# Kernel tuning notes

Hardware: AMD Instinct MI355X
Metric: run time of the kernel (lower is better)

Reference implementation:

```python
import jax, jax.numpy as jnp
import numpy as np

N = 50000      # nodes
DEG = 16       # fixed neighbor count per node -> E = N*DEG edges
F_IN = 128
F_OUT = 128


def setup_inputs() -> dict:
    key = jax.random.key(0)
    k = jax.random.split(key, 6)
    E = N * DEG
    x = jax.random.normal(k[0], (N, F_IN), dtype=jnp.float32)
    weight = jax.random.normal(k[1], (F_IN, F_OUT), dtype=jnp.float32) * (1.0 / np.sqrt(F_OUT))
    bias = jax.random.normal(k[2], (F_OUT,), dtype=jnp.float32) * (1.0 / np.sqrt(F_OUT))
    weights_mask = jax.random.normal(k[3], (2 * F_IN, F_IN), dtype=jnp.float32) * (1.0 / np.sqrt(F_IN))
    adj_vals = jax.random.uniform(k[4], (E,), dtype=jnp.float32)
    edge_src = jax.random.randint(k[5], (E,), 0, N, dtype=jnp.int32)   # neighbor ids (add_all flattened)
    edge_dst = jnp.repeat(jnp.arange(N, dtype=jnp.int32), DEG)         # center node ids
    return {"x": x, "weight": weight, "bias": bias, "weights_mask": weights_mask,
            "adj_vals": adj_vals, "edge_src": edge_src, "edge_dst": edge_dst}


def reference(x, weight, bias, weights_mask, adj_vals, edge_src, edge_dst):
    # Per-edge: concat(center, neighbor) -> mask MLP -> sigmoid (dropout omitted: eval mode)
    cen = x[edge_dst]                    # [E, F]
    nei = x[edge_src]                    # [E, F]
    cen_nei = jnp.concatenate([cen, nei], axis=1)          # [E, 2F]
    mask = jax.nn.sigmoid(cen_nei @ weights_mask)          # [E, F]
    # Weighted neighbor sum scattered back to centers, plus self feature
    agg = jax.ops.segment_sum(mask * nei, edge_dst, num_segments=N)   # [N, F]
    x_new = x + agg
    # Dense transform then spmm aggregation (adj given as edge list with values)
    support = x_new @ weight                                # [N, F_out]
    out = jax.ops.segment_sum(adj_vals[:, None] * support[edge_src], edge_dst, num_segments=N)
    return out + bias
```

## Files before the change

kernel.cpp:

```cpp
#include <hip/hip_runtime.h>
#include <stdint.h>
#include <stddef.h>


#define NNODES 50000
#define DEG    16
#define FD     128

#define NEG_LOG2E -1.44269504f

typedef __bf16 bf16x8 __attribute__((ext_vector_type(8)));
typedef short  s16x8  __attribute__((ext_vector_type(8)));
typedef float  f32x4  __attribute__((ext_vector_type(4)));
typedef float  f32x2  __attribute__((ext_vector_type(2)));

__device__ __forceinline__ short f2bf_s(float f) {
    union { float f; uint32_t u; } v; v.f = f;
    uint32_t r = v.u + 0x7fffu + ((v.u >> 16) & 1u);
    return (short)(r >> 16);
}
__device__ __forceinline__ float bflo(uint32_t u) {
    union { uint32_t u; float f; } v; v.u = u << 16;
    return v.f;
}
__device__ __forceinline__ float bfhi(uint32_t u) {
    union { uint32_t u; float f; } v; v.u = u & 0xffff0000u;
    return v.f;
}
__device__ __forceinline__ uint32_t pkbf(float lo, float hi) {
    return (uint32_t)(uint16_t)f2bf_s(lo) | ((uint32_t)(uint16_t)f2bf_s(hi) << 16);
}

__global__ __launch_bounds__(256) void pack_k(const float* __restrict__ wm,
                                              const float* __restrict__ w,
                                              short* __restrict__ wmb,
                                              short* __restrict__ wpack) {
    int tid = blockIdx.x * 256 + threadIdx.x;
    if (tid < 128 * 256) {
        int k = tid >> 8, c = tid & 255;
        float v = (c < 128) ? wm[k * 128 + c] : wm[(128 + k) * 128 + (c - 128)];
        int idx = (((k >> 5) * 16 + (c >> 4)) * 64 + ((k >> 3) & 3) * 16 + (c & 15)) * 8 + (k & 7);
        wmb[idx] = f2bf_s(NEG_LOG2E * v);
    }
    if (tid < 128 * 128) {
        int k = tid >> 7, n = tid & 127;
        int idx = (((k >> 5) * 8 + (n >> 4)) * 64 + ((k >> 3) & 3) * 16 + (n & 15)) * 8 + (k & 7);
        wpack[idx] = f2bf_s(w[tid]);
    }
}

__global__ __launch_bounds__(256) void zy_k(const float* __restrict__ x,
                                            const short* __restrict__ wmb,
                                            short* __restrict__ ezb,
                                            uint32_t* __restrict__ xb,
                                            uint8_t* __restrict__ y8) {
    __shared__ float ct[16 * 260];
    const int tid = threadIdx.x, wave = tid >> 6, lane = tid & 63;
    const int q = lane >> 4, m = lane & 15;
    const int node0 = blockIdx.x * 16;

    f32x4 acc[4];
    #pragma unroll
    for (int nt = 0; nt < 4; ++nt) acc[nt] = (f32x4){0.f, 0.f, 0.f, 0.f};

    #pragma unroll
    for (int kk = 0; kk < 4; ++kk) {
        const float* rp = x + (size_t)(node0 + m) * FD + kk * 32 + q * 8;
        f32x4 lo = *reinterpret_cast<const f32x4*>(rp);
        f32x4 hi = *reinterpret_cast<const f32x4*>(rp + 4);
        bf16x8 a;
        a[0]=(__bf16)lo.x; a[1]=(__bf16)lo.y; a[2]=(__bf16)lo.z; a[3]=(__bf16)lo.w;
        a[4]=(__bf16)hi.x; a[5]=(__bf16)hi.y; a[6]=(__bf16)hi.z; a[7]=(__bf16)hi.w;
        #pragma unroll
        for (int nt = 0; nt < 4; ++nt) {
            int frag = kk * 16 + wave * 4 + nt;
            s16x8 braw = *reinterpret_cast<const s16x8*>(wmb + ((size_t)frag * 64 + lane) * 8);
            acc[nt] = __builtin_amdgcn_mfma_f32_16x16x32_bf16(a, __builtin_bit_cast(bf16x8, braw), acc[nt], 0, 0, 0);
        }
    }
    #pragma unroll
    for (int nt = 0; nt < 4; ++nt)
        #pragma unroll
        for (int i = 0; i < 4; ++i)
            ct[(q * 4 + i) * 260 + wave * 64 + nt * 16 + m] = acc[nt][i];
    __syncthreads();

    const int row = tid >> 4;
    const int c0  = (tid & 15) * 16;
    const int grow = node0 + row;
    if (c0 < 128) {
        uint32_t zo[8];
        #pragma unroll
        for (int j = 0; j < 8; ++j) {
            float v0 = __builtin_amdgcn_exp2f(ct[row * 260 + c0 + 2 * j]);
            float v1 = __builtin_amdgcn_exp2f(ct[row * 260 + c0 + 2 * j + 1]);
            zo[j] = pkbf(v0, v1);
        }
        uint4* dst = reinterpret_cast<uint4*>(ezb + (size_t)grow * FD + c0);
        dst[0] = make_uint4(zo[0], zo[1], zo[2], zo[3]);
        dst[1] = make_uint4(zo[4], zo[5], zo[6], zo[7]);
    } else {
        const int f0 = c0 - 128;
        const float* xr = x + (size_t)grow * FD + f0;
        uint32_t xo[8];
        #pragma unroll
        for (int j = 0; j < 8; ++j) {
            float v0 = xr[2 * j], v1 = xr[2 * j + 1];
            xo[j] = pkbf(v0, v1);
        }
        uint4* xdst = reinterpret_cast<uint4*>(xb + (size_t)grow * 64 + f0 / 2);
        xdst[0] = make_uint4(xo[0], xo[1], xo[2], xo[3]);
        xdst[1] = make_uint4(xo[4], xo[5], xo[6], xo[7]);
        uint32_t yo[4];
        #pragma unroll
        for (int g = 0; g < 4; ++g) {
            float y0 = __builtin_amdgcn_exp2f(ct[row * 260 + c0 + 4 * g]);
            float y1 = __builtin_amdgcn_exp2f(ct[row * 260 + c0 + 4 * g + 1]);
            float y2 = __builtin_amdgcn_exp2f(ct[row * 260 + c0 + 4 * g + 2]);
            float y3 = __builtin_amdgcn_exp2f(ct[row * 260 + c0 + 4 * g + 3]);
            int u = __builtin_amdgcn_cvt_pk_fp8_f32(y0, y1, 0, false);
            u     = __builtin_amdgcn_cvt_pk_fp8_f32(y2, y3, u, true);
            yo[g] = (uint32_t)u;
        }
        *reinterpret_cast<uint4*>(y8 + (size_t)grow * 128 + f0) = make_uint4(yo[0], yo[1], yo[2], yo[3]);
    }
}

__global__ __launch_bounds__(256) void edge_k(const short* __restrict__ ezb,
                                              const uint32_t* __restrict__ xb,
                                              const uint8_t* __restrict__ y8,
                                              const int* __restrict__ esrc,
                                              uint32_t* __restrict__ xnb) {
    const int tid = threadIdx.x, wave = tid >> 6, lane = tid & 63;
    const int q = lane >> 4, li = lane & 15;
    const int n0 = __builtin_amdgcn_readfirstlane(blockIdx.x * 16 + wave * 4);
    const int nd = n0 + q;

    const int4* ep = reinterpret_cast<const int4*>(esrc + nd * DEG);
    const int4 s0 = ep[0], s1 = ep[1], s2 = ep[2], s3 = ep[3];

    const uint4 ez = *reinterpret_cast<const uint4*>(
        reinterpret_cast<const uint32_t*>(ezb) + (size_t)nd * 64 + li * 4);
    const uint4 cw = *reinterpret_cast<const uint4*>(xb + (size_t)nd * 64 + li * 4);

    uint4 xw0, xw1, xw2, xw3, xw4, xw5, xw6, xw7, xw8, xw9, xw10, xw11, xw12, xw13, xw14, xw15;
    uint2 yw0, yw1, yw2, yw3, yw4, yw5, yw6, yw7, yw8, yw9, yw10, yw11, yw12, yw13, yw14, yw15;
#define LD(I, S) \
    xw##I = *reinterpret_cast<const uint4*>(xb + (size_t)(S) * 64 + li * 4); \
    yw##I = *reinterpret_cast<const uint2*>(y8 + (size_t)(S) * 128 + li * 8);
    LD(0, s0.x)  LD(1, s0.y)  LD(2, s0.z)  LD(3, s0.w)
    LD(4, s1.x)  LD(5, s1.y)  LD(6, s1.z)  LD(7, s1.w)
    LD(8, s2.x)  LD(9, s2.y)  LD(10, s2.z) LD(11, s2.w)
    LD(12, s3.x) LD(13, s3.y) LD(14, s3.z) LD(15, s3.w)
#undef LD

    const float Ez0 = bflo(ez.x), Ez1 = bfhi(ez.x), Ez2 = bflo(ez.y), Ez3 = bfhi(ez.y),
                Ez4 = bflo(ez.z), Ez5 = bfhi(ez.z), Ez6 = bflo(ez.w), Ez7 = bfhi(ez.w);
    float a0 = 0.f, a1 = 0.f, a2 = 0.f, a3 = 0.f, a4 = 0.f, a5 = 0.f, a6 = 0.f, a7 = 0.f;
#define ACC(I) { \
    f32x2 p0 = __builtin_amdgcn_cvt_pk_f32_fp8((int)yw##I.x, false); \
    f32x2 p1 = __builtin_amdgcn_cvt_pk_f32_fp8((int)yw##I.x, true);  \
    f32x2 p2 = __builtin_amdgcn_cvt_pk_f32_fp8((int)yw##I.y, false); \
    f32x2 p3 = __builtin_amdgcn_cvt_pk_f32_fp8((int)yw##I.y, true);  \
    a0 = __builtin_fmaf(__builtin_amdgcn_rcpf(__builtin_fmaf(Ez0, p0.x, 1.f)), bflo(xw##I.x), a0); \
    a1 = __builtin_fmaf(__builtin_amdgcn_rcpf(__builtin_fmaf(Ez1, p0.y, 1.f)), bfhi(xw##I.x), a1); \
    a2 = __builtin_fmaf(__builtin_amdgcn_rcpf(__builtin_fmaf(Ez2, p1.x, 1.f)), bflo(xw##I.y), a2); \
    a3 = __builtin_fmaf(__builtin_amdgcn_rcpf(__builtin_fmaf(Ez3, p1.y, 1.f)), bfhi(xw##I.y), a3); \
    a4 = __builtin_fmaf(__builtin_amdgcn_rcpf(__builtin_fmaf(Ez4, p2.x, 1.f)), bflo(xw##I.z), a4); \
    a5 = __builtin_fmaf(__builtin_amdgcn_rcpf(__builtin_fmaf(Ez5, p2.y, 1.f)), bfhi(xw##I.z), a5); \
    a6 = __builtin_fmaf(__builtin_amdgcn_rcpf(__builtin_fmaf(Ez6, p3.x, 1.f)), bflo(xw##I.w), a6); \
    a7 = __builtin_fmaf(__builtin_amdgcn_rcpf(__builtin_fmaf(Ez7, p3.y, 1.f)), bfhi(xw##I.w), a7); }
    ACC(0)  ACC(1)  ACC(2)  ACC(3)
    ACC(4)  ACC(5)  ACC(6)  ACC(7)
    ACC(8)  ACC(9)  ACC(10) ACC(11)
    ACC(12) ACC(13) ACC(14) ACC(15)
#undef ACC

    const uint32_t o0 = pkbf(bflo(cw.x) + a0, bfhi(cw.x) + a1);
    const uint32_t o1 = pkbf(bflo(cw.y) + a2, bfhi(cw.y) + a3);
    const uint32_t o2 = pkbf(bflo(cw.z) + a4, bfhi(cw.z) + a5);
    const uint32_t o3 = pkbf(bflo(cw.w) + a6, bfhi(cw.w) + a7);
    *reinterpret_cast<uint4*>(xnb + (size_t)nd * 64 + li * 4) = make_uint4(o0, o1, o2, o3);
}

__global__ __launch_bounds__(256) void out_k(const uint32_t* __restrict__ xnb,
                                             const float* __restrict__ adj,
                                             const int* __restrict__ esrc,
                                             const short* __restrict__ wpack,
                                             const float* __restrict__ bias,
                                             float* __restrict__ out) {
    __shared__ float xn[16 * 132];
    const int tid = threadIdx.x, wave = tid >> 6, lane = tid & 63;
    const int q = lane >> 4, m = lane & 15;
    const int li = m;
    const int node0 = blockIdx.x * 16;
    const int n0 = __builtin_amdgcn_readfirstlane(node0 + wave * 4);
    const int nd = n0 + q;

    const int4* ep = reinterpret_cast<const int4*>(esrc + nd * DEG);
    const int4 s0 = ep[0], s1 = ep[1], s2 = ep[2], s3 = ep[3];
    const float4* ap = reinterpret_cast<const float4*>(adj + nd * DEG);
    const float4 w0 = ap[0], w1 = ap[1], w2 = ap[2], w3 = ap[3];

    uint4 u0, u1, u2, u3, u4, u5, u6, u7, u8, u9, u10, u11, u12, u13, u14, u15;
#define LD(I, S) u##I = *reinterpret_cast<const uint4*>(xnb + (size_t)(S) * 64 + li * 4);
    LD(0, s0.x)  LD(1, s0.y)  LD(2, s0.z)  LD(3, s0.w)
    LD(4, s1.x)  LD(5, s1.y)  LD(6, s1.z)  LD(7, s1.w)
    LD(8, s2.x)  LD(9, s2.y)  LD(10, s2.z) LD(11, s2.w)
    LD(12, s3.x) LD(13, s3.y) LD(14, s3.z) LD(15, s3.w)
#undef LD

    float a0 = 0.f, a1 = 0.f, a2 = 0.f, a3 = 0.f, a4 = 0.f, a5 = 0.f, a6 = 0.f, a7 = 0.f;
#define ACC(I, W) \
    a0 = __builtin_fmaf(W, bflo(u##I.x), a0); a1 = __builtin_fmaf(W, bfhi(u##I.x), a1); \
    a2 = __builtin_fmaf(W, bflo(u##I.y), a2); a3 = __builtin_fmaf(W, bfhi(u##I.y), a3); \
    a4 = __builtin_fmaf(W, bflo(u##I.z), a4); a5 = __builtin_fmaf(W, bfhi(u##I.z), a5); \
    a6 = __builtin_fmaf(W, bflo(u##I.w), a6); a7 = __builtin_fmaf(W, bfhi(u##I.w), a7);
    ACC(0, w0.x)  ACC(1, w0.y)  ACC(2, w0.z)  ACC(3, w0.w)
    ACC(4, w1.x)  ACC(5, w1.y)  ACC(6, w1.z)  ACC(7, w1.w)
    ACC(8, w2.x)  ACC(9, w2.y)  ACC(10, w2.z) ACC(11, w2.w)
    ACC(12, w3.x) ACC(13, w3.y) ACC(14, w3.z) ACC(15, w3.w)
#undef ACC

    const int r = wave * 4 + q;
    *reinterpret_cast<f32x4*>(&xn[r * 132 + li * 8])     = (f32x4){a0, a1, a2, a3};
    *reinterpret_cast<f32x4*>(&xn[r * 132 + li * 8 + 4]) = (f32x4){a4, a5, a6, a7};
    __syncthreads();

    f32x4 sacc[2];
    sacc[0] = (f32x4){0.f, 0.f, 0.f, 0.f};
    sacc[1] = (f32x4){0.f, 0.f, 0.f, 0.f};
    #pragma unroll
    for (int kk = 0; kk < 4; ++kk) {
        const float* p = &xn[m * 132 + kk * 32 + q * 8];
        bf16x8 a;
        a[0]=(__bf16)p[0]; a[1]=(__bf16)p[1]; a[2]=(__bf16)p[2]; a[3]=(__bf16)p[3];
        a[4]=(__bf16)p[4]; a[5]=(__bf16)p[5]; a[6]=(__bf16)p[6]; a[7]=(__bf16)p[7];
        #pragma unroll
        for (int t = 0; t < 2; ++t) {
            int nt = wave * 2 + t;
            s16x8 braw = *reinterpret_cast<const s16x8*>(wpack + ((size_t)(kk * 8 + nt) * 64 + lane) * 8);
            sacc[t] = __builtin_amdgcn_mfma_f32_16x16x32_bf16(a, __builtin_bit_cast(bf16x8, braw), sacc[t], 0, 0, 0);
        }
    }
    #pragma unroll
    for (int t = 0; t < 2; ++t) {
        const int f = (wave * 2 + t) * 16 + m;
        const float bv = bias[f];
        #pragma unroll
        for (int i = 0; i < 4; ++i)
            out[(size_t)(node0 + q * 4 + i) * FD + f] = sacc[t][i] + bv;
    }
}

extern "C" void kernel_launch(void* const* d_in, const int* in_sizes, int n_in,
                              void* d_out, int out_size, void* d_ws, size_t ws_size,
                              hipStream_t stream) {
    const float* x      = (const float*)d_in[0];
    const float* weight = (const float*)d_in[1];
    const float* bias   = (const float*)d_in[2];
    const float* wm     = (const float*)d_in[3];
    const float* adj    = (const float*)d_in[4];
    const int*   esrc   = (const int*)d_in[5];

    short*    wmb   = (short*)d_ws;
    short*    wpack = (short*)((char*)d_ws + 65536);
    short*    ezb   = (short*)((char*)d_ws + 98304);
    uint32_t* xnb   = (uint32_t*)((char*)d_ws + 98304 + (size_t)NNODES * FD * 2);
    uint32_t* xb    = (uint32_t*)d_out;
    uint8_t*  y8    = (uint8_t*)d_out + (size_t)NNODES * FD * 2;
    float*    out   = (float*)d_out;

    pack_k <<<128,         256, 0, stream>>>(wm, weight, wmb, wpack);
    zy_k   <<<NNODES / 16, 256, 0, stream>>>(x, wmb, ezb, xb, y8);
    edge_k <<<NNODES / 16, 256, 0, stream>>>(ezb, xb, y8, esrc, xnb);
    out_k  <<<NNODES / 16, 256, 0, stream>>>(xnb, adj, esrc, wpack, bias, out);
}
```

Measured before the change: 181.5 us.

## Slice features into eight column chunks so gathers hit a smaller working set

Intermediate node features (ez, x bf16, y fp8, x_new) are stored feature-sliced: eight separate arrays of 16 features per node. The gather kernels now launch one block per (node chunk, slice) with blockIdx low bits selecting the slice, so concurrently running blocks gather from a single compact slice that fits better in L2/MALL. The final stage is split: agg_k does the spmm gather into a bf16 aggregate buffer, and a separate sup_k applies the weight matmul and bias. This relies on linearity to aggregate before the transform, at the cost of an extra kernel launch, an extra bf16 buffer round trip, and smaller per-lane loads.

```diff
diff --git a/kernel.cpp b/kernel.cpp
--- a/kernel.cpp
+++ b/kernel.cpp
@@ -6,6 +6,7 @@
 #define NNODES 50000
 #define DEG    16
 #define FD     128
+#define NCHUNK 782
 
 #define NEG_LOG2E -1.44269504f
 
@@ -51,9 +52,9 @@
 
 __global__ __launch_bounds__(256) void zy_k(const float* __restrict__ x,
                                             const short* __restrict__ wmb,
-                                            short* __restrict__ ezb,
-                                            uint32_t* __restrict__ xb,
-                                            uint8_t* __restrict__ y8) {
+                                            uint32_t* __restrict__ ezt,
+                                            uint32_t* __restrict__ xbt,
+                                            uint32_t* __restrict__ y8t) {
     __shared__ float ct[16 * 260];
     const int tid = threadIdx.x, wave = tid >> 6, lane = tid & 63;
     const int q = lane >> 4, m = lane & 15;
@@ -89,6 +90,7 @@
     const int c0  = (tid & 15) * 16;
     const int grow = node0 + row;
     if (c0 < 128) {
+        const int s = c0 >> 4;
         uint32_t zo[8];
         #pragma unroll
         for (int j = 0; j < 8; ++j) {
@@ -96,11 +98,11 @@
             float v1 = __builtin_amdgcn_exp2f(ct[row * 260 + c0 + 2 * j + 1]);
             zo[j] = pkbf(v0, v1);
         }
-        uint4* dst = reinterpret_cast<uint4*>(ezb + (size_t)grow * FD + c0);
+        uint4* dst = reinterpret_cast<uint4*>(ezt + (size_t)s * (NNODES * 8) + (size_t)grow * 8);
         dst[0] = make_uint4(zo[0], zo[1], zo[2], zo[3]);
         dst[1] = make_uint4(zo[4], zo[5], zo[6], zo[7]);
     } else {
-        const int f0 = c0 - 128;
+        const int f0 = c0 - 128, s = f0 >> 4;
         const float* xr = x + (size_t)grow * FD + f0;
         uint32_t xo[8];
         #pragma unroll
@@ -108,7 +110,7 @@
             float v0 = xr[2 * j], v1 = xr[2 * j + 1];
             xo[j] = pkbf(v0, v1);
         }
-        uint4* xdst = reinterpret_cast<uint4*>(xb + (size_t)grow * 64 + f0 / 2);
+        uint4* xdst = reinterpret_cast<uint4*>(xbt + (size_t)s * (NNODES * 8) + (size_t)grow * 8);
         xdst[0] = make_uint4(xo[0], xo[1], xo[2], xo[3]);
         xdst[1] = make_uint4(xo[4], xo[5], xo[6], xo[7]);
         uint32_t yo[4];
@@ -122,125 +124,132 @@
             u     = __builtin_amdgcn_cvt_pk_fp8_f32(y2, y3, u, true);
             yo[g] = (uint32_t)u;
         }
-        *reinterpret_cast<uint4*>(y8 + (size_t)grow * 128 + f0) = make_uint4(yo[0], yo[1], yo[2], yo[3]);
-    }
-}
-
-__global__ __launch_bounds__(256) void edge_k(const short* __restrict__ ezb,
-                                              const uint32_t* __restrict__ xb,
-                                              const uint8_t* __restrict__ y8,
+        *reinterpret_cast<uint4*>(y8t + (size_t)s * (NNODES * 4) + (size_t)grow * 4) =
+            make_uint4(yo[0], yo[1], yo[2], yo[3]);
+    }
+}
+
+__global__ __launch_bounds__(256) void edge_k(const uint32_t* __restrict__ ezt,
+                                              const uint32_t* __restrict__ xbt,
+                                              const uint32_t* __restrict__ y8t,
                                               const int* __restrict__ esrc,
-                                              uint32_t* __restrict__ xnb) {
-    const int tid = threadIdx.x, wave = tid >> 6, lane = tid & 63;
-    const int q = lane >> 4, li = lane & 15;
-    const int n0 = __builtin_amdgcn_readfirstlane(blockIdx.x * 16 + wave * 4);
-    const int nd = n0 + q;
+                                              uint32_t* __restrict__ xnt) {
+    const int tid = threadIdx.x, wave = tid >> 6, lane = tid & 63;
+    const int s = blockIdx.x & 7, chunk = blockIdx.x >> 3;
+    const int d = lane >> 2, li = lane & 3;
+    int nd = chunk * 64 + wave * 16 + d;
+    const bool valid = nd < NNODES;
+    nd = valid ? nd : (NNODES - 1);
+
+    const uint32_t* xs = xbt + (size_t)s * (NNODES * 8);
+    const uint32_t* ys = y8t + (size_t)s * (NNODES * 4);
+    const uint32_t* es = ezt + (size_t)s * (NNODES * 8);
+    uint32_t*       os = xnt + (size_t)s * (NNODES * 8);
 
     const int4* ep = reinterpret_cast<const int4*>(esrc + nd * DEG);
-    const int4 s0 = ep[0], s1 = ep[1], s2 = ep[2], s3 = ep[3];
-
-    const uint4 ez = *reinterpret_cast<const uint4*>(
-        reinterpret_cast<const uint32_t*>(ezb) + (size_t)nd * 64 + li * 4);
-    const uint4 cw = *reinterpret_cast<const uint4*>(xb + (size_t)nd * 64 + li * 4);
-
-    uint4 xw0, xw1, xw2, xw3, xw4, xw5, xw6, xw7, xw8, xw9, xw10, xw11, xw12, xw13, xw14, xw15;
-    uint2 yw0, yw1, yw2, yw3, yw4, yw5, yw6, yw7, yw8, yw9, yw10, yw11, yw12, yw13, yw14, yw15;
+    const int4 e0 = ep[0], e1 = ep[1], e2 = ep[2], e3 = ep[3];
+
+    const uint2 ez = *reinterpret_cast<const uint2*>(es + (size_t)nd * 8 + li * 2);
+    const uint2 cw = *reinterpret_cast<const uint2*>(xs + (size_t)nd * 8 + li * 2);
+
+    uint2 xw0, xw1, xw2, xw3, xw4, xw5, xw6, xw7, xw8, xw9, xw10, xw11, xw12, xw13, xw14, xw15;
+    uint32_t yw0, yw1, yw2, yw3, yw4, yw5, yw6, yw7, yw8, yw9, yw10, yw11, yw12, yw13, yw14, yw15;
 #define LD(I, S) \
-    xw##I = *reinterpret_cast<const uint4*>(xb + (size_t)(S) * 64 + li * 4); \
-    yw##I = *reinterpret_cast<const uint2*>(y8 + (size_t)(S) * 128 + li * 8);
-    LD(0, s0.x)  LD(1, s0.y)  LD(2, s0.z)  LD(3, s0.w)
-    LD(4, s1.x)  LD(5, s1.y)  LD(6, s1.z)  LD(7, s1.w)
-    LD(8, s2.x)  LD(9, s2.y)  LD(10, s2.z) LD(11, s2.w)
-    LD(12, s3.x) LD(13, s3.y) LD(14, s3.z) LD(15, s3.w)
+    xw##I = *reinterpret_cast<const uint2*>(xs + (size_t)(S) * 8 + li * 2); \
+    yw##I = ys[(size_t)(S) * 4 + li];
+    LD(0, e0.x)  LD(1, e0.y)  LD(2, e0.z)  LD(3, e0.w)
+    LD(4, e1.x)  LD(5, e1.y)  LD(6, e1.z)  LD(7, e1.w)
+    LD(8, e2.x)  LD(9, e2.y)  LD(10, e2.z) LD(11, e2.w)
+    LD(12, e3.x) LD(13, e3.y) LD(14, e3.z) LD(15, e3.w)
 #undef LD
 
-    const float Ez0 = bflo(ez.x), Ez1 = bfhi(ez.x), Ez2 = bflo(ez.y), Ez3 = bfhi(ez.y),
-                Ez4 = bflo(ez.z), Ez5 = bfhi(ez.z), Ez6 = bflo(ez.w), Ez7 = bfhi(ez.w);
-    float a0 = 0.f, a1 = 0.f, a2 = 0.f, a3 = 0.f, a4 = 0.f, a5 = 0.f, a6 = 0.f, a7 = 0.f;
+    const float Ez0 = bflo(ez.x), Ez1 = bfhi(ez.x), Ez2 = bflo(ez.y), Ez3 = bfhi(ez.y);
+    float a0 = 0.f, a1 = 0.f, a2 = 0.f, a3 = 0.f;
 #define ACC(I) { \
-    f32x2 p0 = __builtin_amdgcn_cvt_pk_f32_fp8((int)yw##I.x, false); \
-    f32x2 p1 = __builtin_amdgcn_cvt_pk_f32_fp8((int)yw##I.x, true);  \
-    f32x2 p2 = __builtin_amdgcn_cvt_pk_f32_fp8((int)yw##I.y, false); \
-    f32x2 p3 = __builtin_amdgcn_cvt_pk_f32_fp8((int)yw##I.y, true);  \
-    a0 = __builtin_fmaf(__builtin_amdgcn_rcpf(__builtin_fmaf(Ez0, p0.x, 1.f)), bflo(xw##I.x), a0); \
-    a1 = __builtin_fmaf(__builtin_amdgcn_rcpf(__builtin_fmaf(Ez1, p0.y, 1.f)), bfhi(xw##I.x), a1); \
-    a2 = __builtin_fmaf(__builtin_amdgcn_rcpf(__builtin_fmaf(Ez2, p1.x, 1.f)), bflo(xw##I.y), a2); \
-    a3 = __builtin_fmaf(__builtin_amdgcn_rcpf(__builtin_fmaf(Ez3, p1.y, 1.f)), bfhi(xw##I.y), a3); \
-    a4 = __builtin_fmaf(__builtin_amdgcn_rcpf(__builtin_fmaf(Ez4, p2.x, 1.f)), bflo(xw##I.z), a4); \
-    a5 = __builtin_fmaf(__builtin_amdgcn_rcpf(__builtin_fmaf(Ez5, p2.y, 1.f)), bfhi(xw##I.z), a5); \
-    a6 = __builtin_fmaf(__builtin_amdgcn_rcpf(__builtin_fmaf(Ez6, p3.x, 1.f)), bflo(xw##I.w), a6); \
-    a7 = __builtin_fmaf(__builtin_amdgcn_rcpf(__builtin_fmaf(Ez7, p3.y, 1.f)), bfhi(xw##I.w), a7); }
+    f32x2 p01 = __builtin_amdgcn_cvt_pk_f32_fp8((int)yw##I, false); \
+    f32x2 p23 = __builtin_amdgcn_cvt_pk_f32_fp8((int)yw##I, true);  \
+    a0 = __builtin_fmaf(__builtin_amdgcn_rcpf(__builtin_fmaf(Ez0, p01.x, 1.f)), bflo(xw##I.x), a0); \
+    a1 = __builtin_fmaf(__builtin_amdgcn_rcpf(__builtin_fmaf(Ez1, p01.y, 1.f)), bfhi(xw##I.x), a1); \
+    a2 = __builtin_fmaf(__builtin_amdgcn_rcpf(__builtin_fmaf(Ez2, p23.x, 1.f)), bflo(xw##I.y), a2); \
+    a3 = __builtin_fmaf(__builtin_amdgcn_rcpf(__builtin_fmaf(Ez3, p23.y, 1.f)), bfhi(xw##I.y), a3); }
     ACC(0)  ACC(1)  ACC(2)  ACC(3)
     ACC(4)  ACC(5)  ACC(6)  ACC(7)
     ACC(8)  ACC(9)  ACC(10) ACC(11)
     ACC(12) ACC(13) ACC(14) ACC(15)
 #undef ACC
 
-    const uint32_t o0 = pkbf(bflo(cw.x) + a0, bfhi(cw.x) + a1);
-    const uint32_t o1 = pkbf(bflo(cw.y) + a2, bfhi(cw.y) + a3);
-    const uint32_t o2 = pkbf(bflo(cw.z) + a4, bfhi(cw.z) + a5);
-    const uint32_t o3 = pkbf(bflo(cw.w) + a6, bfhi(cw.w) + a7);
-    *reinterpret_cast<uint4*>(xnb + (size_t)nd * 64 + li * 4) = make_uint4(o0, o1, o2, o3);
-}
-
-__global__ __launch_bounds__(256) void out_k(const uint32_t* __restrict__ xnb,
+    if (valid) {
+        uint2 o;
+        o.x = pkbf(bflo(cw.x) + a0, bfhi(cw.x) + a1);
+        o.y = pkbf(bflo(cw.y) + a2, bfhi(cw.y) + a3);
+        *reinterpret_cast<uint2*>(os + (size_t)nd * 8 + li * 2) = o;
+    }
+}
+
+__global__ __launch_bounds__(256) void agg_k(const uint32_t* __restrict__ xnt,
                                              const float* __restrict__ adj,
                                              const int* __restrict__ esrc,
-                                             const short* __restrict__ wpack,
-                                             const float* __restrict__ bias,
-                                             float* __restrict__ out) {
-    __shared__ float xn[16 * 132];
-    const int tid = threadIdx.x, wave = tid >> 6, lane = tid & 63;
-    const int q = lane >> 4, m = lane & 15;
-    const int li = m;
-    const int node0 = blockIdx.x * 16;
-    const int n0 = __builtin_amdgcn_readfirstlane(node0 + wave * 4);
-    const int nd = n0 + q;
+                                             uint32_t* __restrict__ aggb) {
+    const int tid = threadIdx.x, wave = tid >> 6, lane = tid & 63;
+    const int s = blockIdx.x & 7, chunk = blockIdx.x >> 3;
+    const int d = lane >> 2, li = lane & 3;
+    int nd = chunk * 64 + wave * 16 + d;
+    const bool valid = nd < NNODES;
+    nd = valid ? nd : (NNODES - 1);
+
+    const uint32_t* xs = xnt + (size_t)s * (NNODES * 8);
 
     const int4* ep = reinterpret_cast<const int4*>(esrc + nd * DEG);
-    const int4 s0 = ep[0], s1 = ep[1], s2 = ep[2], s3 = ep[3];
+    const int4 e0 = ep[0], e1 = ep[1], e2 = ep[2], e3 = ep[3];
     const float4* ap = reinterpret_cast<const float4*>(adj + nd * DEG);
     const float4 w0 = ap[0], w1 = ap[1], w2 = ap[2], w3 = ap[3];
 
-    uint4 u0, u1, u2, u3, u4, u5, u6, u7, u8, u9, u10, u11, u12, u13, u14, u15;
-#define LD(I, S) u##I = *reinterpret_cast<const uint4*>(xnb + (size_t)(S) * 64 + li * 4);
-    LD(0, s0.x)  LD(1, s0.y)  LD(2, s0.z)  LD(3, s0.w)
-    LD(4, s1.x)  LD(5, s1.y)  LD(6, s1.z)  LD(7, s1.w)
-    LD(8, s2.x)  LD(9, s2.y)  LD(10, s2.z) LD(11, s2.w)
-    LD(12, s3.x) LD(13, s3.y) LD(14, s3.z) LD(15, s3.w)
+    uint2 u0, u1, u2, u3, u4, u5, u6, u7, u8, u9, u10, u11, u12, u13, u14, u15;
+#define LD(I, S) u##I = *reinterpret_cast<const uint2*>(xs + (size_t)(S) * 8 + li * 2);
+    LD(0, e0.x)  LD(1, e0.y)  LD(2, e0.z)  LD(3, e0.w)
+    LD(4, e1.x)  LD(5, e1.y)  LD(6, e1.z)  LD(7, e1.w)
+    LD(8, e2.x)  LD(9, e2.y)  LD(10, e2.z) LD(11, e2.w)
+    LD(12, e3.x) LD(13, e3.y) LD(14, e3.z) LD(15, e3.w)
 #undef LD
 
-    float a0 = 0.f, a1 = 0.f, a2 = 0.f, a3 = 0.f, a4 = 0.f, a5 = 0.f, a6 = 0.f, a7 = 0.f;
+    float a0 = 0.f, a1 = 0.f, a2 = 0.f, a3 = 0.f;
 #define ACC(I, W) \
     a0 = __builtin_fmaf(W, bflo(u##I.x), a0); a1 = __builtin_fmaf(W, bfhi(u##I.x), a1); \
-    a2 = __builtin_fmaf(W, bflo(u##I.y), a2); a3 = __builtin_fmaf(W, bfhi(u##I.y), a3); \
-    a4 = __builtin_fmaf(W, bflo(u##I.z), a4); a5 = __builtin_fmaf(W, bfhi(u##I.z), a5); \
-    a6 = __builtin_fmaf(W, bflo(u##I.w), a6); a7 = __builtin_fmaf(W, bfhi(u##I.w), a7);
+    a2 = __builtin_fmaf(W, bflo(u##I.y), a2); a3 = __builtin_fmaf(W, bfhi(u##I.y), a3);
     ACC(0, w0.x)  ACC(1, w0.y)  ACC(2, w0.z)  ACC(3, w0.w)
     ACC(4, w1.x)  ACC(5, w1.y)  ACC(6, w1.z)  ACC(7, w1.w)
     ACC(8, w2.x)  ACC(9, w2.y)  ACC(10, w2.z) ACC(11, w2.w)
     ACC(12, w3.x) ACC(13, w3.y) ACC(14, w3.z) ACC(15, w3.w)
 #undef ACC
 
-    const int r = wave * 4 + q;
-    *reinterpret_cast<f32x4*>(&xn[r * 132 + li * 8])     = (f32x4){a0, a1, a2, a3};
-    *reinterpret_cast<f32x4*>(&xn[r * 132 + li * 8 + 4]) = (f32x4){a4, a5, a6, a7};
-    __syncthreads();
+    if (valid) {
+        uint2 o;
+        o.x = pkbf(a0, a1);
+        o.y = pkbf(a2, a3);
+        *reinterpret_cast<uint2*>(aggb + (size_t)nd * 64 + s * 8 + li * 2) = o;
+    }
+}
+
+__global__ __launch_bounds__(256) void sup_k(const short* __restrict__ aggb,
+                                             const short* __restrict__ wpack,
+                                             const float* __restrict__ bias,
+                                             float* __restrict__ out) {
+    const int tid = threadIdx.x, wave = tid >> 6, lane = tid & 63;
+    const int q = lane >> 4, m = lane & 15;
+    const int node0 = blockIdx.x * 16;
 
     f32x4 sacc[2];
     sacc[0] = (f32x4){0.f, 0.f, 0.f, 0.f};
     sacc[1] = (f32x4){0.f, 0.f, 0.f, 0.f};
     #pragma unroll
     for (int kk = 0; kk < 4; ++kk) {
-        const float* p = &xn[m * 132 + kk * 32 + q * 8];
-        bf16x8 a;
-        a[0]=(__bf16)p[0]; a[1]=(__bf16)p[1]; a[2]=(__bf16)p[2]; a[3]=(__bf16)p[3];
-        a[4]=(__bf16)p[4]; a[5]=(__bf16)p[5]; a[6]=(__bf16)p[6]; a[7]=(__bf16)p[7];
+        s16x8 araw = *reinterpret_cast<const s16x8*>(aggb + (size_t)(node0 + m) * FD + kk * 32 + q * 8);
         #pragma unroll
         for (int t = 0; t < 2; ++t) {
             int nt = wave * 2 + t;
             s16x8 braw = *reinterpret_cast<const s16x8*>(wpack + ((size_t)(kk * 8 + nt) * 64 + lane) * 8);
-            sacc[t] = __builtin_amdgcn_mfma_f32_16x16x32_bf16(a, __builtin_bit_cast(bf16x8, braw), sacc[t], 0, 0, 0);
+            sacc[t] = __builtin_amdgcn_mfma_f32_16x16x32_bf16(
+                __builtin_bit_cast(bf16x8, araw), __builtin_bit_cast(bf16x8, braw), sacc[t], 0, 0, 0);
         }
     }
     #pragma unroll
@@ -263,16 +272,19 @@
     const float* adj    = (const float*)d_in[4];
     const int*   esrc   = (const int*)d_in[5];
 
+    const size_t SLICED = (size_t)NNODES * FD * 2;
     short*    wmb   = (short*)d_ws;
     short*    wpack = (short*)((char*)d_ws + 65536);
-    short*    ezb   = (short*)((char*)d_ws + 98304);
-    uint32_t* xnb   = (uint32_t*)((char*)d_ws + 98304 + (size_t)NNODES * FD * 2);
-    uint32_t* xb    = (uint32_t*)d_out;
-    uint8_t*  y8    = (uint8_t*)d_out + (size_t)NNODES * FD * 2;
+    uint32_t* ezt   = (uint32_t*)((char*)d_ws + 98304);
+    uint32_t* xnt   = (uint32_t*)((char*)d_ws + 98304 + SLICED);
+    uint32_t* aggb  = (uint32_t*)((char*)d_ws + 98304 + 2 * SLICED);
+    uint32_t* xbt   = (uint32_t*)d_out;
+    uint32_t* y8t   = (uint32_t*)((char*)d_out + SLICED);
     float*    out   = (float*)d_out;
 
     pack_k <<<128,         256, 0, stream>>>(wm, weight, wmb, wpack);
-    zy_k   <<<NNODES / 16, 256, 0, stream>>>(x, wmb, ezb, xb, y8);
-    edge_k <<<NNODES / 16, 256, 0, stream>>>(ezb, xb, y8, esrc, xnb);
-    out_k  <<<NNODES / 16, 256, 0, stream>>>(xnb, adj, esrc, wpack, bias, out);
-}
+    zy_k   <<<NNODES / 16, 256, 0, stream>>>(x, wmb, ezt, xbt, y8t);
+    edge_k <<<NCHUNK * 8,  256, 0, stream>>>(ezt, xbt, y8t, esrc, xnt);
+    agg_k  <<<NCHUNK * 8,  256, 0, stream>>>(xnt, adj, esrc, aggb);
+    sup_k  <<<NNODES / 16, 256, 0, stream>>>((const short*)aggb, wpack, bias, out);
+}
```

New measurement: 218.9 us. +20.6%, slower.
